# Kernel optimization log

Hardware: AMD Instinct MI355X
Metric: run time of the kernel (lower is better)

Reference implementation:

```python
import jax, jax.numpy as jnp
import numpy as np

N_STEPS = 20  # ceil((t1-t0)/dt0) with dt0=0.05 on [0,1]


def setup_inputs() -> dict:
    key = jax.random.key(0)
    ks = jax.random.split(key, 12)
    B, D, H, VF, LS, LAB = 512, 5, 128, 256, 63, 10
    Lm1 = LS - 1  # 62, effective logsig dim after dropping channel 0
    ts = jnp.linspace(0.0, 1.0, 33, dtype=jnp.float32)
    intervals = jnp.linspace(0.0, 1.0, 33, dtype=jnp.float32)
    logsig = jax.random.normal(ks[0], (32, LS), dtype=jnp.float32)
    x0 = jax.random.normal(ks[1], (B, D), dtype=jnp.float32)
    def lin(k, fan_in, shape):
        return jax.random.uniform(k, shape, jnp.float32, -1.0, 1.0) / np.sqrt(fan_in)
    return {
        "ts": ts, "logsig": logsig, "x0": x0, "intervals": intervals,
        "W_vf1": lin(ks[2], H, (VF, H)),  "b_vf1": lin(ks[3], H, (VF,)),
        "W_vf2": lin(ks[4], VF, (VF, VF)), "b_vf2": lin(ks[5], VF, (VF,)),
        "W_m": lin(ks[6], VF, (H * Lm1, VF)), "b_m": lin(ks[7], VF, (H * Lm1,)),
        "W_in": lin(ks[8], D, (H, D)),   "b_in": lin(ks[9], D, (H,)),
        "W_out": lin(ks[10], H, (LAB, H)), "b_out": lin(ks[11], H, (LAB,)),
    }


def reference(ts, logsig, x0, intervals, W_vf1, b_vf1, W_vf2, b_vf2,
              W_m, b_m, W_in, b_in, W_out, b_out):
    B = x0.shape[0]
    H = W_in.shape[0]
    L = logsig.shape[1] - 1  # channel 0 dropped

    def vector_field(t, y):
        # locate interval containing t (torch.searchsorted default = left)
        idx = jnp.clip(jnp.searchsorted(intervals[1:], t) + 1, 1, intervals.shape[0] - 1)
        seg = logsig[idx - 1, 1:]                     # (L,)
        h = jax.nn.relu(y @ W_vf1.T + b_vf1)          # (B, VF)
        h = jnp.tanh(h @ W_vf2.T + b_vf2)             # (B, VF) final_activation=tanh
        m = (h @ W_m.T + b_m).reshape(B, H, L)        # (B, H, L)
        dydt = jnp.einsum('bhl,l->bh', m, seg)
        return dydt / (intervals[idx] - intervals[idx - 1])

    y0 = x0 @ W_in.T + b_in                           # linear1
    t0, t1 = ts[0], ts[-1]
    dt = (t1 - t0) / N_STEPS

    def heun_step(y, i):
        t = t0 + i * dt
        k1 = vector_field(t, y)
        k2 = vector_field(t + dt, y + dt * k1)
        return y + 0.5 * dt * (k1 + k2), None

    yT, _ = jax.lax.scan(heun_step, y0, jnp.arange(N_STEPS, dtype=jnp.float32))
    return jax.nn.softmax(yT @ W_out.T + b_out, axis=-1)
```

## Files before the change

### kernel.cpp

```cpp
#include <hip/hip_runtime.h>

#define YW 136

typedef _Float16 f16x8 __attribute__((ext_vector_type(8)));
typedef _Float16 f16x4 __attribute__((ext_vector_type(4)));
typedef __attribute__((ext_vector_type(4))) float f32x4;

__device__ __forceinline__ float fast_tanh(float x) {
    float e = __expf(2.0f * x);
    return 1.0f - 2.0f / (e + 1.0f);
}
__device__ __forceinline__ void bar_lds() {
    asm volatile("s_waitcnt lgkmcnt(0)\n\ts_barrier" ::: "memory");
}

__device__ __forceinline__ int fidx(int m, int c) {
    return ((c >> 5) << 9) | (((c >> 3) & 3) << 7) | (m << 3) | (c & 7);
}

__global__ __launch_bounds__(256) void pk_all(
    const float* __restrict__ Wvf1, const float* __restrict__ Wvf2,
    const float* __restrict__ Wm,   const float* __restrict__ bm,
    const float* __restrict__ logsig,
    _Float16* __restrict__ W1F, _Float16* __restrict__ W2F,
    _Float16* __restrict__ A3F, float* __restrict__ c_all)
{
    __shared__ float ls[32][62];
    const int b = blockIdx.x, t = threadIdx.x;
    if (b < 128) {
        int u = b * 256 + t;
        int j = u & 7, l = (u >> 3) & 63;
        int kc = (u >> 9) & 3, nt = (u >> 9) >> 2;
        int n = nt * 16 + (l & 15), k = kc * 32 + (l >> 4) * 8 + j;
        float w = Wvf1[n * 128 + k];
        _Float16 hi = (_Float16)w;
        W1F[u] = hi;
        W1F[32768 + u] = (_Float16)(w - (float)hi);
    } else if (b < 384) {
        int u = (b - 128) * 256 + t;
        int j = u & 7, l = (u >> 3) & 63;
        int kc = (u >> 9) & 7, nt = (u >> 9) >> 3;
        int n = nt * 16 + (l & 15), k = kc * 32 + (l >> 4) * 8 + j;
        float w = Wvf2[n * 256 + k];
        _Float16 hi = (_Float16)w;
        W2F[u] = hi;
        W2F[65536 + u] = (_Float16)(w - (float)hi);
    } else if (b < 896) {
        for (int e2 = t; e2 < 32 * 62; e2 += 256)
            ls[e2 / 62][e2 % 62] = logsig[(e2 / 62) * 63 + 1 + (e2 % 62)];
        __syncthreads();
        int idx = b - 384;
        int chunk = idx >> 7;
        int u = (idx & 127) * 256 + t;
        int j = u & 7, l = (u >> 3) & 63, kc = (u >> 9) & 7, nt = (u >> 12) & 7;
        int h = nt * 16 + (l & 15);
        int v = kc * 32 + (l >> 4) * 8 + j;
        int r0 = chunk * 8;
        float acc[8];
#pragma unroll
        for (int r = 0; r < 8; r++) acc[r] = 0.f;
#pragma unroll
        for (int ll = 0; ll < 62; ll++) {
            float wv2 = Wm[(h * 62 + ll) * 256 + v];
#pragma unroll
            for (int r = 0; r < 8; r++) acc[r] += wv2 * ls[r0 + r][ll];
        }
#pragma unroll
        for (int r = 0; r < 8; r++) {
            _Float16 hi = (_Float16)acc[r];
            A3F[(r0 + r) * 65536 + u] = hi;
            A3F[(r0 + r) * 65536 + 32768 + u] = (_Float16)(acc[r] - (float)hi);
        }
    } else {
        int u = (b - 896) * 256 + t;
        int r = u >> 7, h = u & 127;
        float acc = 0.f;
#pragma unroll
        for (int ll = 0; ll < 62; ll++) acc += bm[h * 62 + ll] * logsig[r * 63 + 1 + ll];
        c_all[u] = acc;
    }
}

__global__ __launch_bounds__(512, 2) void rde_main(
    const float* __restrict__ ts, const float* __restrict__ x0,
    const float* __restrict__ intervals,
    const float* __restrict__ b1g, const float* __restrict__ b2g,
    const float* __restrict__ Win, const float* __restrict__ bin,
    const float* __restrict__ Wout, const float* __restrict__ bout,
    const _Float16* __restrict__ W1F, const _Float16* __restrict__ W2F,
    const _Float16* __restrict__ A3F, const float* __restrict__ c_all,
    float* __restrict__ out)
{
    __shared__ __align__(16) _Float16 W1s[65536];
    __shared__ __align__(16) _Float16 HBUF[2][4096];
    __shared__ __align__(16) _Float16 YBUF[2][2048];
    __shared__ float ivl[33];
    __shared__ int   r_arr[40];
    __shared__ float s_arr[40];

    _Float16* Hh = HBUF[0];
    _Float16* Hl = HBUF[1];
    _Float16* Yh = YBUF[0];
    _Float16* Yl = YBUF[1];

    const int t    = threadIdx.x;
    const int lane = t & 63;
    const int wv   = t >> 6;
    const int m16  = lane & 15;
    const int q    = lane >> 4;
    const int row0 = blockIdx.x * 16;

    if (t < 33) ivl[t] = intervals[t];
    for (int e2 = t; e2 < 8192; e2 += 512)
        ((uint4*)W1s)[e2] = ((const uint4*)W1F)[e2];
    __syncthreads();

    const float ts0 = ts[0];
    const float dt  = __fdiv_rn(ts[32] - ts0, 20.0f);

    if (t < 40) {
        int i = t >> 1;
        float tv = ts0 + (float)i * dt;
        if (t & 1) tv += dt;
        int p = 0;
        for (int j2 = 0; j2 < 32; j2++) p += (ivl[1 + j2] < tv) ? 1 : 0;
        int idx = p + 1;
        idx = idx < 1 ? 1 : idx;
        idx = idx > 32 ? 32 : idx;
        r_arr[t] = idx - 1;
        s_arr[t] = __fdiv_rn(1.0f, ivl[idx] - ivl[idx - 1]);
    }

    f32x4 b1f[2], b2f[2];
#pragma unroll
    for (int tt = 0; tt < 2; tt++) {
        b1f[tt] = *(const f32x4*)(b1g + (wv * 2 + tt) * 16 + q * 4);
        b2f[tt] = *(const f32x4*)(b2g + (wv * 2 + tt) * 16 + q * 4);
    }

    float Y[4], K1[4];
    {
        const float* xr = x0 + (row0 + m16) * 5;
        float xv[5];
#pragma unroll
        for (int d = 0; d < 5; d++) xv[d] = xr[d];
        int c0 = wv * 16 + q * 4;
        f16x4 hv, lv;
#pragma unroll
        for (int r = 0; r < 4; r++) {
            float acc = bin[c0 + r];
#pragma unroll
            for (int d = 0; d < 5; d++) acc += xv[d] * Win[(c0 + r) * 5 + d];
            Y[r] = acc;
            K1[r] = 0.f;
            _Float16 hi = (_Float16)acc;
            hv[r] = hi;
            lv[r] = (_Float16)(acc - (float)hi);
        }
        *(f16x4*)(Yh + fidx(m16, c0)) = hv;
        *(f16x4*)(Yl + fidx(m16, c0)) = lv;
    }
    __syncthreads();

#pragma unroll 1
    for (int e = 0; e < 40; e++) {
        const int half = e & 1;
        const int ri   = r_arr[e];
        const float s  = s_arr[e];
        const _Float16* ABase = A3F + ri * 65536;

        f16x8 w2a[2][4][2];
#pragma unroll
        for (int tt = 0; tt < 2; tt++)
#pragma unroll
            for (int kc = 0; kc < 4; kc++) {
                const _Float16* bp = W2F + ((wv * 16 + tt * 8 + kc) * 64 + lane) * 8;
                w2a[tt][kc][0] = *(const f16x8*)bp;
                w2a[tt][kc][1] = *(const f16x8*)(bp + 65536);
            }
        f32x4 aA[2], aB[2], aC[2];
#pragma unroll
        for (int tt = 0; tt < 2; tt++) {
            aA[tt] = b1f[tt];
            aB[tt] = (f32x4){0.f, 0.f, 0.f, 0.f};
            aC[tt] = (f32x4){0.f, 0.f, 0.f, 0.f};
        }
#pragma unroll
        for (int kc = 0; kc < 4; kc++) {
            f16x8 ah = *(const f16x8*)(Yh + kc * 512 + lane * 8);
            f16x8 al = *(const f16x8*)(Yl + kc * 512 + lane * 8);
#pragma unroll
            for (int tt = 0; tt < 2; tt++) {
                int wb = ((wv * 8 + tt * 4 + kc) * 64 + lane) * 8;
                f16x8 bh = *(const f16x8*)(W1s + wb);
                f16x8 bl = *(const f16x8*)(W1s + 32768 + wb);
                aA[tt] = __builtin_amdgcn_mfma_f32_16x16x32_f16(bh, ah, aA[tt], 0, 0, 0);
                aB[tt] = __builtin_amdgcn_mfma_f32_16x16x32_f16(bl, ah, aB[tt], 0, 0, 0);
                aC[tt] = __builtin_amdgcn_mfma_f32_16x16x32_f16(bh, al, aC[tt], 0, 0, 0);
            }
        }
#pragma unroll
        for (int tt = 0; tt < 2; tt++) {
            int n0 = (wv * 2 + tt) * 16 + q * 4;
            f16x4 hv, lv;
#pragma unroll
            for (int r = 0; r < 4; r++) {
                float v = fmaxf(aA[tt][r] + aB[tt][r] + aC[tt][r], 0.f);
                _Float16 hi = (_Float16)v;
                hv[r] = hi;
                lv[r] = (_Float16)(v - (float)hi);
            }
            *(f16x4*)(Hh + fidx(m16, n0)) = hv;
            *(f16x4*)(Hl + fidx(m16, n0)) = lv;
        }
        bar_lds();

        f16x8 w2b[2][4][2];
#pragma unroll
        for (int tt = 0; tt < 2; tt++)
#pragma unroll
            for (int kc = 0; kc < 4; kc++) {
                const _Float16* bp = W2F + ((wv * 16 + tt * 8 + 4 + kc) * 64 + lane) * 8;
                w2b[tt][kc][0] = *(const f16x8*)bp;
                w2b[tt][kc][1] = *(const f16x8*)(bp + 65536);
            }
#pragma unroll
        for (int tt = 0; tt < 2; tt++) {
            aA[tt] = b2f[tt];
            aB[tt] = (f32x4){0.f, 0.f, 0.f, 0.f};
            aC[tt] = (f32x4){0.f, 0.f, 0.f, 0.f};
        }
#pragma unroll
        for (int kc = 0; kc < 4; kc++) {
            f16x8 ah = *(const f16x8*)(Hh + kc * 512 + lane * 8);
            f16x8 al = *(const f16x8*)(Hl + kc * 512 + lane * 8);
#pragma unroll
            for (int tt = 0; tt < 2; tt++) {
                aA[tt] = __builtin_amdgcn_mfma_f32_16x16x32_f16(w2a[tt][kc][0], ah, aA[tt], 0, 0, 0);
                aB[tt] = __builtin_amdgcn_mfma_f32_16x16x32_f16(w2a[tt][kc][1], ah, aB[tt], 0, 0, 0);
                aC[tt] = __builtin_amdgcn_mfma_f32_16x16x32_f16(w2a[tt][kc][0], al, aC[tt], 0, 0, 0);
            }
        }
        f16x8 a3a[4][2];
#pragma unroll
        for (int kc = 0; kc < 4; kc++) {
            const _Float16* bp = ABase + ((wv * 8 + kc) * 64 + lane) * 8;
            a3a[kc][0] = *(const f16x8*)bp;
            a3a[kc][1] = *(const f16x8*)(bp + 32768);
        }
        f32x4 cf = *(const f32x4*)(c_all + ri * 128 + wv * 16 + q * 4);
#pragma unroll
        for (int kc = 0; kc < 4; kc++) {
            f16x8 ah = *(const f16x8*)(Hh + (4 + kc) * 512 + lane * 8);
            f16x8 al = *(const f16x8*)(Hl + (4 + kc) * 512 + lane * 8);
#pragma unroll
            for (int tt = 0; tt < 2; tt++) {
                aA[tt] = __builtin_amdgcn_mfma_f32_16x16x32_f16(w2b[tt][kc][0], ah, aA[tt], 0, 0, 0);
                aB[tt] = __builtin_amdgcn_mfma_f32_16x16x32_f16(w2b[tt][kc][1], ah, aB[tt], 0, 0, 0);
                aC[tt] = __builtin_amdgcn_mfma_f32_16x16x32_f16(w2b[tt][kc][0], al, aC[tt], 0, 0, 0);
            }
        }
        f16x8 a3b[4][2];
#pragma unroll
        for (int kc = 0; kc < 4; kc++) {
            const _Float16* bp = ABase + ((wv * 8 + 4 + kc) * 64 + lane) * 8;
            a3b[kc][0] = *(const f16x8*)bp;
            a3b[kc][1] = *(const f16x8*)(bp + 32768);
        }
        bar_lds();
#pragma unroll
        for (int tt = 0; tt < 2; tt++) {
            int n0 = (wv * 2 + tt) * 16 + q * 4;
            f16x4 hv, lv;
#pragma unroll
            for (int r = 0; r < 4; r++) {
                float v = fast_tanh(aA[tt][r] + aB[tt][r] + aC[tt][r]);
                _Float16 hi = (_Float16)v;
                hv[r] = hi;
                lv[r] = (_Float16)(v - (float)hi);
            }
            *(f16x4*)(Hh + fidx(m16, n0)) = hv;
            *(f16x4*)(Hl + fidx(m16, n0)) = lv;
        }
        bar_lds();

        f32x4 kA = cf;
        f32x4 kB = (f32x4){0.f, 0.f, 0.f, 0.f};
        f32x4 kC = (f32x4){0.f, 0.f, 0.f, 0.f};
#pragma unroll
        for (int kc = 0; kc < 4; kc++) {
            f16x8 ah = *(const f16x8*)(Hh + kc * 512 + lane * 8);
            f16x8 al = *(const f16x8*)(Hl + kc * 512 + lane * 8);
            kA = __builtin_amdgcn_mfma_f32_16x16x32_f16(a3a[kc][0], ah, kA, 0, 0, 0);
            kB = __builtin_amdgcn_mfma_f32_16x16x32_f16(a3a[kc][1], ah, kB, 0, 0, 0);
            kC = __builtin_amdgcn_mfma_f32_16x16x32_f16(a3a[kc][0], al, kC, 0, 0, 0);
        }
#pragma unroll
        for (int kc = 0; kc < 4; kc++) {
            f16x8 ah = *(const f16x8*)(Hh + (4 + kc) * 512 + lane * 8);
            f16x8 al = *(const f16x8*)(Hl + (4 + kc) * 512 + lane * 8);
            kA = __builtin_amdgcn_mfma_f32_16x16x32_f16(a3b[kc][0], ah, kA, 0, 0, 0);
            kB = __builtin_amdgcn_mfma_f32_16x16x32_f16(a3b[kc][1], ah, kB, 0, 0, 0);
            kC = __builtin_amdgcn_mfma_f32_16x16x32_f16(a3b[kc][0], al, kC, 0, 0, 0);
        }
        {
            int c0 = wv * 16 + q * 4;
            f16x4 hv, lv;
#pragma unroll
            for (int r = 0; r < 4; r++) {
                float kv = (kA[r] + kB[r] + kC[r]) * s;
                float yn;
                if (half == 0) {
                    K1[r] = kv;
                    yn = Y[r] + dt * kv;
                } else {
                    yn = Y[r] + 0.5f * dt * (K1[r] + kv);
                    Y[r] = yn;
                }
                _Float16 hi = (_Float16)yn;
                hv[r] = hi;
                lv[r] = (_Float16)(yn - (float)hi);
            }
            *(f16x4*)(Yh + fidx(m16, c0)) = hv;
            *(f16x4*)(Yl + fidx(m16, c0)) = lv;
        }
        bar_lds();
    }

    float* Ys  = (float*)&HBUF[0][0];
    float* lgp = (float*)&HBUF[0][0] + 16 * YW;
#pragma unroll
    for (int r = 0; r < 4; r++)
        Ys[m16 * YW + wv * 16 + q * 4 + r] = Y[r];
    __syncthreads();
    if (t < 160) {
        int m = t / 10, c = t % 10;
        float acc = bout[c];
        for (int k = 0; k < 128; k++) acc += Ys[m * YW + k] * Wout[c * 128 + k];
        lgp[m * 10 + c] = acc;
    }
    __syncthreads();
    if (t < 16) {
        float mx = -1e30f;
#pragma unroll
        for (int c = 0; c < 10; c++) mx = fmaxf(mx, lgp[t * 10 + c]);
        float ex[10], sum = 0.f;
#pragma unroll
        for (int c = 0; c < 10; c++) { ex[c] = expf(lgp[t * 10 + c] - mx); sum += ex[c]; }
        float inv = __fdiv_rn(1.0f, sum);
#pragma unroll
        for (int c = 0; c < 10; c++) out[(row0 + t) * 10 + c] = ex[c] * inv;
    }
}

extern "C" void kernel_launch(void* const* d_in, const int* in_sizes, int n_in,
                              void* d_out, int out_size, void* d_ws, size_t ws_size,
                              hipStream_t stream) {
    const float* ts     = (const float*)d_in[0];
    const float* logsig = (const float*)d_in[1];
    const float* x0     = (const float*)d_in[2];
    const float* ivls   = (const float*)d_in[3];
    const float* Wvf1   = (const float*)d_in[4];
    const float* bvf1   = (const float*)d_in[5];
    const float* Wvf2   = (const float*)d_in[6];
    const float* bvf2   = (const float*)d_in[7];
    const float* Wm     = (const float*)d_in[8];
    const float* bm     = (const float*)d_in[9];
    const float* Win    = (const float*)d_in[10];
    const float* bin    = (const float*)d_in[11];
    const float* Wout   = (const float*)d_in[12];
    const float* bout   = (const float*)d_in[13];

    _Float16* W1F = (_Float16*)d_ws;
    _Float16* W2F = W1F + 65536;
    _Float16* A3F = W2F + 131072;
    float* c_all = (float*)(A3F + 32 * 65536);
    float* out = (float*)d_out;

    pk_all<<<dim3(912), dim3(256), 0, stream>>>(Wvf1, Wvf2, Wm, bm, logsig,
                                                W1F, W2F, A3F, c_all);
    rde_main<<<dim3(32), dim3(512), 0, stream>>>(
        ts, x0, ivls, bvf1, bvf2, Win, bin, Wout, bout,
        W1F, W2F, A3F, c_all, out);
}
```

Before: 254.2 us.

## Drop low-half activation split for hidden layers and move W1 low part to registers

Hidden activations h1 and h2 are stored as single fp16 values instead of hi/lo split pairs, which removes the third MFMA correction term in the W2 and W_m matmuls. The W1 low-precision half moves from LDS into registers, reloaded from global memory each step. Separate H1/H2 buffers remove one barrier per step. LDS use drops by about half. The cost is lower accuracy of the hidden activations and higher register pressure, which could cut occupancy under launch_bounds(512,2).

```diff
diff --git a/kernel.cpp b/kernel.cpp
--- a/kernel.cpp
+++ b/kernel.cpp
@@ -91,17 +91,14 @@
     const _Float16* __restrict__ A3F, const float* __restrict__ c_all,
     float* __restrict__ out)
 {
-    __shared__ __align__(16) _Float16 W1s[65536];
-    __shared__ __align__(16) _Float16 HBUF[2][4096];
-    __shared__ __align__(16) _Float16 YBUF[2][2048];
+    __shared__ __align__(16) _Float16 W1s[32768];
+    __shared__ __align__(16) _Float16 H1h[4096];
+    __shared__ __align__(16) _Float16 H2h[4096];
+    __shared__ __align__(16) _Float16 Yh[2048];
+    __shared__ __align__(16) _Float16 Yl[2048];
     __shared__ float ivl[33];
     __shared__ int   r_arr[40];
     __shared__ float s_arr[40];
-
-    _Float16* Hh = HBUF[0];
-    _Float16* Hl = HBUF[1];
-    _Float16* Yh = YBUF[0];
-    _Float16* Yl = YBUF[1];
 
     const int t    = threadIdx.x;
     const int lane = t & 63;
@@ -111,7 +108,7 @@
     const int row0 = blockIdx.x * 16;
 
     if (t < 33) ivl[t] = intervals[t];
-    for (int e2 = t; e2 < 8192; e2 += 512)
+    for (int e2 = t; e2 < 4096; e2 += 512)
         ((uint4*)W1s)[e2] = ((const uint4*)W1F)[e2];
     __syncthreads();
 
@@ -160,6 +157,13 @@
         *(f16x4*)(Yh + fidx(m16, c0)) = hv;
         *(f16x4*)(Yl + fidx(m16, c0)) = lv;
     }
+
+    f16x8 w1lo[2][4];
+#pragma unroll
+    for (int tt = 0; tt < 2; tt++)
+#pragma unroll
+        for (int kc = 0; kc < 4; kc++)
+            w1lo[tt][kc] = *(const f16x8*)(W1F + 32768 + ((wv * 8 + tt * 4 + kc) * 64 + lane) * 8);
     __syncthreads();
 
 #pragma unroll 1
@@ -191,27 +195,20 @@
             f16x8 al = *(const f16x8*)(Yl + kc * 512 + lane * 8);
 #pragma unroll
             for (int tt = 0; tt < 2; tt++) {
-                int wb = ((wv * 8 + tt * 4 + kc) * 64 + lane) * 8;
-                f16x8 bh = *(const f16x8*)(W1s + wb);
-                f16x8 bl = *(const f16x8*)(W1s + 32768 + wb);
+                f16x8 bh = *(const f16x8*)(W1s + ((wv * 8 + tt * 4 + kc) * 64 + lane) * 8);
                 aA[tt] = __builtin_amdgcn_mfma_f32_16x16x32_f16(bh, ah, aA[tt], 0, 0, 0);
-                aB[tt] = __builtin_amdgcn_mfma_f32_16x16x32_f16(bl, ah, aB[tt], 0, 0, 0);
+                aB[tt] = __builtin_amdgcn_mfma_f32_16x16x32_f16(w1lo[tt][kc], ah, aB[tt], 0, 0, 0);
                 aC[tt] = __builtin_amdgcn_mfma_f32_16x16x32_f16(bh, al, aC[tt], 0, 0, 0);
             }
         }
 #pragma unroll
         for (int tt = 0; tt < 2; tt++) {
             int n0 = (wv * 2 + tt) * 16 + q * 4;
-            f16x4 hv, lv;
-#pragma unroll
-            for (int r = 0; r < 4; r++) {
-                float v = fmaxf(aA[tt][r] + aB[tt][r] + aC[tt][r], 0.f);
-                _Float16 hi = (_Float16)v;
-                hv[r] = hi;
-                lv[r] = (_Float16)(v - (float)hi);
-            }
-            *(f16x4*)(Hh + fidx(m16, n0)) = hv;
-            *(f16x4*)(Hl + fidx(m16, n0)) = lv;
+            f16x4 hv;
+#pragma unroll
+            for (int r = 0; r < 4; r++)
+                hv[r] = (_Float16)fmaxf(aA[tt][r] + aB[tt][r] + aC[tt][r], 0.f);
+            *(f16x4*)(H1h + fidx(m16, n0)) = hv;
         }
         bar_lds();
 
@@ -228,17 +225,14 @@
         for (int tt = 0; tt < 2; tt++) {
             aA[tt] = b2f[tt];
             aB[tt] = (f32x4){0.f, 0.f, 0.f, 0.f};
-            aC[tt] = (f32x4){0.f, 0.f, 0.f, 0.f};
-        }
-#pragma unroll
-        for (int kc = 0; kc < 4; kc++) {
-            f16x8 ah = *(const f16x8*)(Hh + kc * 512 + lane * 8);
-            f16x8 al = *(const f16x8*)(Hl + kc * 512 + lane * 8);
+        }
+#pragma unroll
+        for (int kc = 0; kc < 4; kc++) {
+            f16x8 ah = *(const f16x8*)(H1h + kc * 512 + lane * 8);
 #pragma unroll
             for (int tt = 0; tt < 2; tt++) {
                 aA[tt] = __builtin_amdgcn_mfma_f32_16x16x32_f16(w2a[tt][kc][0], ah, aA[tt], 0, 0, 0);
                 aB[tt] = __builtin_amdgcn_mfma_f32_16x16x32_f16(w2a[tt][kc][1], ah, aB[tt], 0, 0, 0);
-                aC[tt] = __builtin_amdgcn_mfma_f32_16x16x32_f16(w2a[tt][kc][0], al, aC[tt], 0, 0, 0);
             }
         }
         f16x8 a3a[4][2];
@@ -251,13 +245,11 @@
         f32x4 cf = *(const f32x4*)(c_all + ri * 128 + wv * 16 + q * 4);
 #pragma unroll
         for (int kc = 0; kc < 4; kc++) {
-            f16x8 ah = *(const f16x8*)(Hh + (4 + kc) * 512 + lane * 8);
-            f16x8 al = *(const f16x8*)(Hl + (4 + kc) * 512 + lane * 8);
+            f16x8 ah = *(const f16x8*)(H1h + (4 + kc) * 512 + lane * 8);
 #pragma unroll
             for (int tt = 0; tt < 2; tt++) {
                 aA[tt] = __builtin_amdgcn_mfma_f32_16x16x32_f16(w2b[tt][kc][0], ah, aA[tt], 0, 0, 0);
                 aB[tt] = __builtin_amdgcn_mfma_f32_16x16x32_f16(w2b[tt][kc][1], ah, aB[tt], 0, 0, 0);
-                aC[tt] = __builtin_amdgcn_mfma_f32_16x16x32_f16(w2b[tt][kc][0], al, aC[tt], 0, 0, 0);
             }
         }
         f16x8 a3b[4][2];
@@ -267,48 +259,42 @@
             a3b[kc][0] = *(const f16x8*)bp;
             a3b[kc][1] = *(const f16x8*)(bp + 32768);
         }
-        bar_lds();
 #pragma unroll
         for (int tt = 0; tt < 2; tt++) {
             int n0 = (wv * 2 + tt) * 16 + q * 4;
-            f16x4 hv, lv;
-#pragma unroll
-            for (int r = 0; r < 4; r++) {
-                float v = fast_tanh(aA[tt][r] + aB[tt][r] + aC[tt][r]);
-                _Float16 hi = (_Float16)v;
-                hv[r] = hi;
-                lv[r] = (_Float16)(v - (float)hi);
-            }
-            *(f16x4*)(Hh + fidx(m16, n0)) = hv;
-            *(f16x4*)(Hl + fidx(m16, n0)) = lv;
+            f16x4 hv;
+#pragma unroll
+            for (int r = 0; r < 4; r++)
+                hv[r] = (_Float16)fast_tanh(aA[tt][r] + aB[tt][r]);
+            *(f16x4*)(H2h + fidx(m16, n0)) = hv;
         }
         bar_lds();
 
         f32x4 kA = cf;
         f32x4 kB = (f32x4){0.f, 0.f, 0.f, 0.f};
-        f32x4 kC = (f32x4){0.f, 0.f, 0.f, 0.f};
-#pragma unroll
-        for (int kc = 0; kc < 4; kc++) {
-            f16x8 ah = *(const f16x8*)(Hh + kc * 512 + lane * 8);
-            f16x8 al = *(const f16x8*)(Hl + kc * 512 + lane * 8);
+#pragma unroll
+        for (int kc = 0; kc < 4; kc++) {
+            f16x8 ah = *(const f16x8*)(H2h + kc * 512 + lane * 8);
             kA = __builtin_amdgcn_mfma_f32_16x16x32_f16(a3a[kc][0], ah, kA, 0, 0, 0);
             kB = __builtin_amdgcn_mfma_f32_16x16x32_f16(a3a[kc][1], ah, kB, 0, 0, 0);
-            kC = __builtin_amdgcn_mfma_f32_16x16x32_f16(a3a[kc][0], al, kC, 0, 0, 0);
-        }
-#pragma unroll
-        for (int kc = 0; kc < 4; kc++) {
-            f16x8 ah = *(const f16x8*)(Hh + (4 + kc) * 512 + lane * 8);
-            f16x8 al = *(const f16x8*)(Hl + (4 + kc) * 512 + lane * 8);
+        }
+#pragma unroll
+        for (int kc = 0; kc < 4; kc++) {
+            f16x8 ah = *(const f16x8*)(H2h + (4 + kc) * 512 + lane * 8);
             kA = __builtin_amdgcn_mfma_f32_16x16x32_f16(a3b[kc][0], ah, kA, 0, 0, 0);
             kB = __builtin_amdgcn_mfma_f32_16x16x32_f16(a3b[kc][1], ah, kB, 0, 0, 0);
-            kC = __builtin_amdgcn_mfma_f32_16x16x32_f16(a3b[kc][0], al, kC, 0, 0, 0);
-        }
+        }
+#pragma unroll
+        for (int tt = 0; tt < 2; tt++)
+#pragma unroll
+            for (int kc = 0; kc < 4; kc++)
+                w1lo[tt][kc] = *(const f16x8*)(W1F + 32768 + ((wv * 8 + tt * 4 + kc) * 64 + lane) * 8);
         {
             int c0 = wv * 16 + q * 4;
             f16x4 hv, lv;
 #pragma unroll
             for (int r = 0; r < 4; r++) {
-                float kv = (kA[r] + kB[r] + kC[r]) * s;
+                float kv = (kA[r] + kB[r]) * s;
                 float yn;
                 if (half == 0) {
                     K1[r] = kv;
@@ -327,8 +313,8 @@
         bar_lds();
     }
 
-    float* Ys  = (float*)&HBUF[0][0];
-    float* lgp = (float*)&HBUF[0][0] + 16 * YW;
+    float* Ys  = (float*)&W1s[0];
+    float* lgp = (float*)&W1s[0] + 16 * YW;
 #pragma unroll
     for (int r = 0; r < 4; r++)
         Ys[m16 * YW + wv * 16 + q * 4 + r] = Y[r];
```

Measured after the change: 239.2 us. 5.9% less time.
